# Performance work log

Hardware: AMD Instinct MI355X
Metric: run time of the kernel (lower is better)

The kernel has to match this reference:

```python
import jax, jax.numpy as jnp
import numpy as np
import itertools

N = 7  # particles per leaf -> 7! = 5040 permutations
PERMS = jnp.array(list(itertools.permutations(range(N))), dtype=jnp.int32)  # (5040, 7)


def _lex_signs(n):
    # signs of n! permutations in lexicographic order, built iteratively as in the source
    s = np.ones(1, dtype=np.float32)
    for i in range(2, n + 1):
        alt = (-1.0) ** np.arange(i)  # alternating signs [1, -1, 1, ...]
        s = np.concatenate([a * s for a in alt])
    return jnp.asarray(s, dtype=jnp.float32)

SIGNS = _lex_signs(N)  # (5040,)


def _antisymmetrize(x, W, b, V, c):
    # x: (B, n, d); fn is MLP (n*d) -> hidden -> dout with tanh
    B, n, d = x.shape
    xp = jnp.take(x, PERMS, axis=-2)                     # (B, n!, n, d)
    xp = xp.reshape(B, PERMS.shape[0], n * d)            # (B, n!, n*d)
    h = jnp.tanh(jnp.einsum('bpf,fh->bph', xp, W) + b)   # (B, n!, H)
    out = jnp.einsum('bph,ho->bpo', h, V) + c            # (B, n!, dout)
    return jnp.sum(SIGNS[:, None] * out, axis=-2)        # (B, dout)


def setup_inputs() -> dict:
    key = jax.random.key(0)
    ks = jax.random.split(key, 6)
    B, n, d, H, O = 128, 7, 16, 128, 1
    f = n * d
    sc_in = 1.0 / np.sqrt(f)
    sc_h = 1.0 / np.sqrt(H)
    return {
        "x0": jax.random.normal(ks[0], (B, n, d), dtype=jnp.float32),
        "x1": jax.random.normal(ks[1], (B, n, d), dtype=jnp.float32),
        "W0": jax.random.normal(ks[2], (f, H), dtype=jnp.float32) * sc_in,
        "b0": jnp.zeros((H,), dtype=jnp.float32),
        "V0": jax.random.normal(ks[3], (H, O), dtype=jnp.float32) * sc_h,
        "c0": jnp.zeros((O,), dtype=jnp.float32),
        "W1": jax.random.normal(ks[4], (f, H), dtype=jnp.float32) * sc_in,
        "b1": jnp.zeros((H,), dtype=jnp.float32),
        "V1": jax.random.normal(ks[5], (H, O), dtype=jnp.float32) * sc_h,
        "c1": jnp.zeros((O,), dtype=jnp.float32),
    }


def reference(x0, x1, W0, b0, V0, c0, W1, b1, V1, c1):
    psi0 = _antisymmetrize(x0, W0, b0, V0, c0)  # (B, 1)
    psi1 = _antisymmetrize(x1, W1, b1, V1, c1)  # (B, 1)
    # logabs=True path: slog multiply over leaves
    sign = jnp.sign(psi0) * jnp.sign(psi1)
    logabs = jnp.log(jnp.abs(psi0)) + jnp.log(jnp.abs(psi1))
    return sign, logabs
```

## Files before the change

### kernel.cpp

```cpp
#include <hip/hip_runtime.h>
#include <math.h>

#define NH 128
#define ND 16
#define NF 112
#define NB 128

#define CC 2.8853900817779268f

typedef float f2 __attribute__((ext_vector_type(2)));

__device__ __forceinline__ float rcpf(float x) { return __builtin_amdgcn_rcpf(x); }

#define GLD(i, j) (*(const f2*)&psh[((i) * 7 + (j)) * NH + (lane << 1)])

#define PAIRP(E4v, Sp, Dp, PMp) do {                              \
    f2 e4 = (E4v);                                                \
    f2 sq = e4 * e4;                                              \
    f2 n  = e4 * (Dp);                                            \
    f2 d;                                                         \
    d.x = fmaf(e4.x, (Sp).x, 1.0f);  d.y = fmaf(e4.y, (Sp).y, 1.0f); \
    d.x = fmaf(sq.x, (PMp).x, d.x);  d.y = fmaf(sq.y, (PMp).y, d.y); \
    f2 rd; rd.x = rcpf(d.x); rd.y = rcpf(d.y);                    \
    accG.x = fmaf(n.x, rd.x, accG.x);                             \
    accG.y = fmaf(n.y, rd.y, accG.y);                             \
  } while (0)

#define PAIRM(E4v, Sp, Dp, PMp) do {                              \
    f2 e4 = (E4v);                                                \
    f2 sq = e4 * e4;                                              \
    f2 n  = e4 * (Dp);                                            \
    f2 d;                                                         \
    d.x = fmaf(e4.x, (Sp).x, 1.0f);  d.y = fmaf(e4.y, (Sp).y, 1.0f); \
    d.x = fmaf(sq.x, (PMp).x, d.x);  d.y = fmaf(sq.y, (PMp).y, d.y); \
    f2 rd; rd.x = rcpf(d.x); rd.y = rcpf(d.y);                    \
    accG.x = fmaf(-n.x, rd.x, accG.x);                            \
    accG.y = fmaf(-n.y, rd.y, accG.y);                            \
  } while (0)

#define T3P(E2v, G3, M4P, M4Q, M4R, S1,D1,PM1, S2,D2,PM2, S3,D3,PM3) do { \
    f2 E3 = (E2v) * (G3);                                         \
    PAIRP(E3 * (M4P), S1, D1, PM1);                               \
    PAIRM(E3 * (M4Q), S2, D2, PM2);                               \
    PAIRP(E3 * (M4R), S3, D3, PM3);                               \
  } while (0)

#define T3M(E2v, G3, M4P, M4Q, M4R, S1,D1,PM1, S2,D2,PM2, S3,D3,PM3) do { \
    f2 E3 = (E2v) * (G3);                                         \
    PAIRM(E3 * (M4P), S1, D1, PM1);                               \
    PAIRP(E3 * (M4Q), S2, D2, PM2);                               \
    PAIRM(E3 * (M4R), S3, D3, PM3);                               \
  } while (0)

#define TRIO(Q2J, TA, TB, g3a, g3b, g3c, g3d, m4a, m4b, m4c, m4d,       \
             Scd,Dcd,PMcd, Sbd,Dbd,PMbd, Sbc,Dbc,PMbc,                  \
             Sad,Dad,PMad, Sac,Dac,PMac, Sab,Dab,PMab) do {             \
    f2 E2 = E1 * (Q2J);                                                 \
    TA(E2, g3a, m4b, m4c, m4d, Scd,Dcd,PMcd, Sbd,Dbd,PMbd, Sbc,Dbc,PMbc); \
    TB(E2, g3b, m4a, m4c, m4d, Scd,Dcd,PMcd, Sad,Dad,PMad, Sac,Dac,PMac); \
    TA(E2, g3c, m4a, m4b, m4d, Sbd,Dbd,PMbd, Sad,Dad,PMad, Sab,Dab,PMab); \
    TB(E2, g3d, m4a, m4b, m4c, Sbc,Dbc,PMbc, Sac,Dac,PMac, Sab,Dab,PMab); \
  } while (0)

#define MKPAIR(X, Y)                                                    \
    f2 S##X##Y, Dd##X##Y, PM##X##Y;                                     \
    {                                                                   \
      f2 P = q5##X * q6##Y;                                             \
      f2 M = q5##Y * q6##X;                                             \
      S##X##Y = P + M; Dd##X##Y = P - M; PM##X##Y = P * M;              \
    }

extern "C" __global__ void __launch_bounds__(512, 4)
antisym_leaf_kernel(const float* __restrict__ x0, const float* __restrict__ x1,
                    const float* __restrict__ W0, const float* __restrict__ b0,
                    const float* __restrict__ V0,
                    const float* __restrict__ W1, const float* __restrict__ b1,
                    const float* __restrict__ V1,
                    float* __restrict__ ws) {
  __shared__ float psh[49 * NH];
  __shared__ float xs[NF];
  __shared__ float red[8];

  const int tid  = threadIdx.x;
  const int bid  = blockIdx.x;
  const int leaf = bid >> 8;
  const int half = (bid >> 7) & 1;
  const int b    = bid & 127;

  const float* xL = leaf ? x1 : x0;
  const float* WL = leaf ? W1 : W0;
  const float* bL = leaf ? b1 : b0;
  const float* vL = leaf ? V1 : V0;

  if (tid < NF) xs[tid] = xL[b * NF + tid];
  __syncthreads();

  for (int idx = tid; idx < 49 * NH; idx += 512) {
    int h  = idx & (NH - 1);
    int ij = idx >> 7;
    int i  = ij / 7;
    int j  = ij - 7 * i;
    const float* wp = WL + i * ND * NH + h;
    const float* xp = xs + j * ND;
    float v = 0.f;
#pragma unroll
    for (int k = 0; k < ND; ++k) v = fmaf(xp[k], wp[k * NH], v);
    psh[idx] = __builtin_amdgcn_exp2f(v * CC);
  }
  __syncthreads();

  const int lane = tid & 63;
  const int wid  = tid >> 6;
  const int slot = (half << 3) | wid;

  f2 bias2 = ((const f2*)bL)[lane];
  f2 V2    = ((const f2*)vL)[lane];
  f2 Eb;
  Eb.x = __builtin_amdgcn_exp2f(bias2.x * CC);
  Eb.y = __builtin_amdgcn_exp2f(bias2.y * CC);
  f2 acc = {0.f, 0.f};

#pragma unroll 1
  for (int k = 0; k < 3; ++k) {
    int g = slot + (k << 4);
    if (g >= 42) break;
    int t0 = g / 6;
    int c1 = g - 6 * t0;
    int t1 = c1 + (c1 >= t0 ? 1 : 0);
    float sg1 = ((t0 + c1) & 1) ? -1.f : 1.f;

    int rm = 0x7F & ~((1 << t0) | (1 << t1));
    int r0 = __ffs(rm) - 1; rm &= rm - 1;
    int r1 = __ffs(rm) - 1; rm &= rm - 1;
    int r2 = __ffs(rm) - 1; rm &= rm - 1;
    int r3 = __ffs(rm) - 1; rm &= rm - 1;
    int r4 = __ffs(rm) - 1;

    f2 E1  = Eb * GLD(0, t0) * GLD(1, t1);
    f2 q20 = GLD(2, r0), q21 = GLD(2, r1), q22 = GLD(2, r2), q23 = GLD(2, r3), q24 = GLD(2, r4);
    f2 g30 = GLD(3, r0), g31 = GLD(3, r1), g32 = GLD(3, r2), g33 = GLD(3, r3), g34 = GLD(3, r4);
    f2 m40 = GLD(4, r0), m41 = GLD(4, r1), m42 = GLD(4, r2), m43 = GLD(4, r3), m44 = GLD(4, r4);
    f2 q50 = GLD(5, r0), q51 = GLD(5, r1), q52 = GLD(5, r2), q53 = GLD(5, r3), q54 = GLD(5, r4);
    f2 q60 = GLD(6, r0), q61 = GLD(6, r1), q62 = GLD(6, r2), q63 = GLD(6, r3), q64 = GLD(6, r4);

    MKPAIR(0, 1) MKPAIR(0, 2) MKPAIR(0, 3) MKPAIR(0, 4)
    MKPAIR(1, 2) MKPAIR(1, 3) MKPAIR(1, 4)
    MKPAIR(2, 3) MKPAIR(2, 4)
    MKPAIR(3, 4)

    f2 accG = {0.f, 0.f};
    TRIO(q20, T3P, T3M, g31, g32, g33, g34, m41, m42, m43, m44,
         S34,Dd34,PM34, S24,Dd24,PM24, S23,Dd23,PM23,
         S14,Dd14,PM14, S13,Dd13,PM13, S12,Dd12,PM12);
    TRIO(q21, T3M, T3P, g30, g32, g33, g34, m40, m42, m43, m44,
         S34,Dd34,PM34, S24,Dd24,PM24, S23,Dd23,PM23,
         S04,Dd04,PM04, S03,Dd03,PM03, S02,Dd02,PM02);
    TRIO(q22, T3P, T3M, g30, g31, g33, g34, m40, m41, m43, m44,
         S34,Dd34,PM34, S14,Dd14,PM14, S13,Dd13,PM13,
         S04,Dd04,PM04, S03,Dd03,PM03, S01,Dd01,PM01);
    TRIO(q23, T3M, T3P, g30, g31, g32, g34, m40, m41, m42, m44,
         S24,Dd24,PM24, S14,Dd14,PM14, S12,Dd12,PM12,
         S04,Dd04,PM04, S02,Dd02,PM02, S01,Dd01,PM01);
    TRIO(q24, T3P, T3M, g30, g31, g32, g33, m40, m41, m42, m43,
         S23,Dd23,PM23, S13,Dd13,PM13, S12,Dd12,PM12,
         S03,Dd03,PM03, S02,Dd02,PM02, S01,Dd01,PM01);

    acc.x = fmaf(sg1, accG.x, acc.x);
    acc.y = fmaf(sg1, accG.y, acc.y);
  }

  float part = V2.x * acc.x + V2.y * acc.y;
#pragma unroll
  for (int off = 32; off > 0; off >>= 1) part += __shfl_xor(part, off, 64);
  if (lane == 0) red[wid] = part;
  __syncthreads();
  if (tid == 0) {
    float tot = 0.f;
#pragma unroll
    for (int w = 0; w < 8; ++w) tot += red[w];
    ws[leaf * 256 + half * 128 + b] = tot;
  }
}

extern "C" __global__ void finalize_kernel(const float* __restrict__ ws,
                                           float* __restrict__ out) {
  int t = threadIdx.x;
  if (t < NB) {
    float p0 = 2.0f * (ws[t] + ws[128 + t]);
    float p1 = 2.0f * (ws[256 + t] + ws[384 + t]);
    float s0 = (p0 > 0.f) ? 1.f : ((p0 < 0.f) ? -1.f : 0.f);
    float s1 = (p1 > 0.f) ? 1.f : ((p1 < 0.f) ? -1.f : 0.f);
    out[t]      = s0 * s1;
    out[NB + t] = logf(fabsf(p0)) + logf(fabsf(p1));
  }
}

extern "C" void kernel_launch(void* const* d_in, const int* in_sizes, int n_in,
                              void* d_out, int out_size, void* d_ws, size_t ws_size,
                              hipStream_t stream) {
  const float* x0 = (const float*)d_in[0];
  const float* x1 = (const float*)d_in[1];
  const float* W0 = (const float*)d_in[2];
  const float* b0 = (const float*)d_in[3];
  const float* V0 = (const float*)d_in[4];
  const float* W1 = (const float*)d_in[6];
  const float* b1 = (const float*)d_in[7];
  const float* V1 = (const float*)d_in[8];

  float* ws  = (float*)d_ws;
  float* out = (float*)d_out;

  antisym_leaf_kernel<<<512, 512, 0, stream>>>(x0, x1, W0, b0, V0, W1, b1, V1, ws);
  finalize_kernel<<<1, NB, 0, stream>>>(ws, out);
}
```

Measured before the change: 31.08 us.

## Split hidden channels across wave pairs and double grid to four splits per leaf

Each lane now handles one hidden channel instead of two packed ones, with pairs of waves covering the 128 channels. The 42 (t0,t1) groups are spread over four block splits per batch row instead of two, so the grid doubles to 1024 blocks. Launch bounds are raised to allow 6 blocks per CU, and finalize sums four partials per leaf. Halving per-thread register state is meant to raise occupancy and parallelism. In exchange, every block recomputes the 49x128 exp table for its row, so that setup work doubles, and the packed f2 arithmetic is given up.

```diff
diff --git a/kernel.cpp b/kernel.cpp
--- a/kernel.cpp
+++ b/kernel.cpp
@@ -8,54 +8,46 @@
 
 #define CC 2.8853900817779268f
 
-typedef float f2 __attribute__((ext_vector_type(2)));
-
 __device__ __forceinline__ float rcpf(float x) { return __builtin_amdgcn_rcpf(x); }
 
-#define GLD(i, j) (*(const f2*)&psh[((i) * 7 + (j)) * NH + (lane << 1)])
-
-#define PAIRP(E4v, Sp, Dp, PMp) do {                              \
-    f2 e4 = (E4v);                                                \
-    f2 sq = e4 * e4;                                              \
-    f2 n  = e4 * (Dp);                                            \
-    f2 d;                                                         \
-    d.x = fmaf(e4.x, (Sp).x, 1.0f);  d.y = fmaf(e4.y, (Sp).y, 1.0f); \
-    d.x = fmaf(sq.x, (PMp).x, d.x);  d.y = fmaf(sq.y, (PMp).y, d.y); \
-    f2 rd; rd.x = rcpf(d.x); rd.y = rcpf(d.y);                    \
-    accG.x = fmaf(n.x, rd.x, accG.x);                             \
-    accG.y = fmaf(n.y, rd.y, accG.y);                             \
-  } while (0)
-
-#define PAIRM(E4v, Sp, Dp, PMp) do {                              \
-    f2 e4 = (E4v);                                                \
-    f2 sq = e4 * e4;                                              \
-    f2 n  = e4 * (Dp);                                            \
-    f2 d;                                                         \
-    d.x = fmaf(e4.x, (Sp).x, 1.0f);  d.y = fmaf(e4.y, (Sp).y, 1.0f); \
-    d.x = fmaf(sq.x, (PMp).x, d.x);  d.y = fmaf(sq.y, (PMp).y, d.y); \
-    f2 rd; rd.x = rcpf(d.x); rd.y = rcpf(d.y);                    \
-    accG.x = fmaf(-n.x, rd.x, accG.x);                            \
-    accG.y = fmaf(-n.y, rd.y, accG.y);                            \
+#define GLD(i, j) (psh[((i) * 7 + (j)) * NH + ch])
+
+#define PAIRP(E4v, Sp, Dp, PMp) do {               \
+    float e4 = (E4v);                              \
+    float sq = e4 * e4;                            \
+    float n  = e4 * (Dp);                          \
+    float d  = fmaf(e4, (Sp), 1.0f);               \
+    d = fmaf(sq, (PMp), d);                        \
+    accG = fmaf(n, rcpf(d), accG);                 \
+  } while (0)
+
+#define PAIRM(E4v, Sp, Dp, PMp) do {               \
+    float e4 = (E4v);                              \
+    float sq = e4 * e4;                            \
+    float n  = e4 * (Dp);                          \
+    float d  = fmaf(e4, (Sp), 1.0f);               \
+    d = fmaf(sq, (PMp), d);                        \
+    accG = fmaf(-n, rcpf(d), accG);                \
   } while (0)
 
 #define T3P(E2v, G3, M4P, M4Q, M4R, S1,D1,PM1, S2,D2,PM2, S3,D3,PM3) do { \
-    f2 E3 = (E2v) * (G3);                                         \
-    PAIRP(E3 * (M4P), S1, D1, PM1);                               \
-    PAIRM(E3 * (M4Q), S2, D2, PM2);                               \
-    PAIRP(E3 * (M4R), S3, D3, PM3);                               \
+    float E3 = (E2v) * (G3);                       \
+    PAIRP(E3 * (M4P), S1, D1, PM1);                \
+    PAIRM(E3 * (M4Q), S2, D2, PM2);                \
+    PAIRP(E3 * (M4R), S3, D3, PM3);                \
   } while (0)
 
 #define T3M(E2v, G3, M4P, M4Q, M4R, S1,D1,PM1, S2,D2,PM2, S3,D3,PM3) do { \
-    f2 E3 = (E2v) * (G3);                                         \
-    PAIRM(E3 * (M4P), S1, D1, PM1);                               \
-    PAIRP(E3 * (M4Q), S2, D2, PM2);                               \
-    PAIRM(E3 * (M4R), S3, D3, PM3);                               \
+    float E3 = (E2v) * (G3);                       \
+    PAIRM(E3 * (M4P), S1, D1, PM1);                \
+    PAIRP(E3 * (M4Q), S2, D2, PM2);                \
+    PAIRM(E3 * (M4R), S3, D3, PM3);                \
   } while (0)
 
 #define TRIO(Q2J, TA, TB, g3a, g3b, g3c, g3d, m4a, m4b, m4c, m4d,       \
              Scd,Dcd,PMcd, Sbd,Dbd,PMbd, Sbc,Dbc,PMbc,                  \
              Sad,Dad,PMad, Sac,Dac,PMac, Sab,Dab,PMab) do {             \
-    f2 E2 = E1 * (Q2J);                                                 \
+    float E2 = E1 * (Q2J);                                              \
     TA(E2, g3a, m4b, m4c, m4d, Scd,Dcd,PMcd, Sbd,Dbd,PMbd, Sbc,Dbc,PMbc); \
     TB(E2, g3b, m4a, m4c, m4d, Scd,Dcd,PMcd, Sad,Dad,PMad, Sac,Dac,PMac); \
     TA(E2, g3c, m4a, m4b, m4d, Sbd,Dbd,PMbd, Sad,Dad,PMad, Sab,Dab,PMab); \
@@ -63,14 +55,14 @@
   } while (0)
 
 #define MKPAIR(X, Y)                                                    \
-    f2 S##X##Y, Dd##X##Y, PM##X##Y;                                     \
+    float S##X##Y, Dd##X##Y, PM##X##Y;                                  \
     {                                                                   \
-      f2 P = q5##X * q6##Y;                                             \
-      f2 M = q5##Y * q6##X;                                             \
+      float P = q5##X * q6##Y;                                          \
+      float M = q5##Y * q6##X;                                          \
       S##X##Y = P + M; Dd##X##Y = P - M; PM##X##Y = P * M;              \
     }
 
-extern "C" __global__ void __launch_bounds__(512, 4)
+extern "C" __global__ void __launch_bounds__(512, 6)
 antisym_leaf_kernel(const float* __restrict__ x0, const float* __restrict__ x1,
                     const float* __restrict__ W0, const float* __restrict__ b0,
                     const float* __restrict__ V0,
@@ -81,11 +73,11 @@
   __shared__ float xs[NF];
   __shared__ float red[8];
 
-  const int tid  = threadIdx.x;
-  const int bid  = blockIdx.x;
-  const int leaf = bid >> 8;
-  const int half = (bid >> 7) & 1;
-  const int b    = bid & 127;
+  const int tid   = threadIdx.x;
+  const int bid   = blockIdx.x;
+  const int leaf  = bid >> 9;
+  const int split = (bid >> 7) & 3;
+  const int b     = bid & 127;
 
   const float* xL = leaf ? x1 : x0;
   const float* WL = leaf ? W1 : W0;
@@ -111,14 +103,12 @@
 
   const int lane = tid & 63;
   const int wid  = tid >> 6;
-  const int slot = (half << 3) | wid;
-
-  f2 bias2 = ((const f2*)bL)[lane];
-  f2 V2    = ((const f2*)vL)[lane];
-  f2 Eb;
-  Eb.x = __builtin_amdgcn_exp2f(bias2.x * CC);
-  Eb.y = __builtin_amdgcn_exp2f(bias2.y * CC);
-  f2 acc = {0.f, 0.f};
+  const int ch   = ((wid & 1) << 6) | lane;
+  const int slot = (split << 2) | (wid >> 1);
+
+  float V1c = vL[ch];
+  float Eb  = __builtin_amdgcn_exp2f(bL[ch] * CC);
+  float acc = 0.f;
 
 #pragma unroll 1
   for (int k = 0; k < 3; ++k) {
@@ -136,19 +126,19 @@
     int r3 = __ffs(rm) - 1; rm &= rm - 1;
     int r4 = __ffs(rm) - 1;
 
-    f2 E1  = Eb * GLD(0, t0) * GLD(1, t1);
-    f2 q20 = GLD(2, r0), q21 = GLD(2, r1), q22 = GLD(2, r2), q23 = GLD(2, r3), q24 = GLD(2, r4);
-    f2 g30 = GLD(3, r0), g31 = GLD(3, r1), g32 = GLD(3, r2), g33 = GLD(3, r3), g34 = GLD(3, r4);
-    f2 m40 = GLD(4, r0), m41 = GLD(4, r1), m42 = GLD(4, r2), m43 = GLD(4, r3), m44 = GLD(4, r4);
-    f2 q50 = GLD(5, r0), q51 = GLD(5, r1), q52 = GLD(5, r2), q53 = GLD(5, r3), q54 = GLD(5, r4);
-    f2 q60 = GLD(6, r0), q61 = GLD(6, r1), q62 = GLD(6, r2), q63 = GLD(6, r3), q64 = GLD(6, r4);
+    float E1  = Eb * GLD(0, t0) * GLD(1, t1);
+    float q20 = GLD(2, r0), q21 = GLD(2, r1), q22 = GLD(2, r2), q23 = GLD(2, r3), q24 = GLD(2, r4);
+    float g30 = GLD(3, r0), g31 = GLD(3, r1), g32 = GLD(3, r2), g33 = GLD(3, r3), g34 = GLD(3, r4);
+    float m40 = GLD(4, r0), m41 = GLD(4, r1), m42 = GLD(4, r2), m43 = GLD(4, r3), m44 = GLD(4, r4);
+    float q50 = GLD(5, r0), q51 = GLD(5, r1), q52 = GLD(5, r2), q53 = GLD(5, r3), q54 = GLD(5, r4);
+    float q60 = GLD(6, r0), q61 = GLD(6, r1), q62 = GLD(6, r2), q63 = GLD(6, r3), q64 = GLD(6, r4);
 
     MKPAIR(0, 1) MKPAIR(0, 2) MKPAIR(0, 3) MKPAIR(0, 4)
     MKPAIR(1, 2) MKPAIR(1, 3) MKPAIR(1, 4)
     MKPAIR(2, 3) MKPAIR(2, 4)
     MKPAIR(3, 4)
 
-    f2 accG = {0.f, 0.f};
+    float accG = 0.f;
     TRIO(q20, T3P, T3M, g31, g32, g33, g34, m41, m42, m43, m44,
          S34,Dd34,PM34, S24,Dd24,PM24, S23,Dd23,PM23,
          S14,Dd14,PM14, S13,Dd13,PM13, S12,Dd12,PM12);
@@ -165,11 +155,10 @@
          S23,Dd23,PM23, S13,Dd13,PM13, S12,Dd12,PM12,
          S03,Dd03,PM03, S02,Dd02,PM02, S01,Dd01,PM01);
 
-    acc.x = fmaf(sg1, accG.x, acc.x);
-    acc.y = fmaf(sg1, accG.y, acc.y);
-  }
-
-  float part = V2.x * acc.x + V2.y * acc.y;
+    acc = fmaf(sg1, accG, acc);
+  }
+
+  float part = V1c * acc;
 #pragma unroll
   for (int off = 32; off > 0; off >>= 1) part += __shfl_xor(part, off, 64);
   if (lane == 0) red[wid] = part;
@@ -178,7 +167,7 @@
     float tot = 0.f;
 #pragma unroll
     for (int w = 0; w < 8; ++w) tot += red[w];
-    ws[leaf * 256 + half * 128 + b] = tot;
+    ws[leaf * 512 + split * 128 + b] = tot;
   }
 }
 
@@ -186,8 +175,8 @@
                                            float* __restrict__ out) {
   int t = threadIdx.x;
   if (t < NB) {
-    float p0 = 2.0f * (ws[t] + ws[128 + t]);
-    float p1 = 2.0f * (ws[256 + t] + ws[384 + t]);
+    float p0 = 2.0f * (ws[t] + ws[128 + t] + ws[256 + t] + ws[384 + t]);
+    float p1 = 2.0f * (ws[512 + t] + ws[640 + t] + ws[768 + t] + ws[896 + t]);
     float s0 = (p0 > 0.f) ? 1.f : ((p0 < 0.f) ? -1.f : 0.f);
     float s1 = (p1 > 0.f) ? 1.f : ((p1 < 0.f) ? -1.f : 0.f);
     out[t]      = s0 * s1;
@@ -210,6 +199,6 @@
   float* ws  = (float*)d_ws;
   float* out = (float*)d_out;
 
-  antisym_leaf_kernel<<<512, 512, 0, stream>>>(x0, x1, W0, b0, V0, W1, b1, V1, ws);
+  antisym_leaf_kernel<<<1024, 512, 0, stream>>>(x0, x1, W0, b0, V0, W1, b1, V1, ws);
   finalize_kernel<<<1, NB, 0, stream>>>(ws, out);
 }
```

New measurement: 49.31 us. 1.59x slower.
